# Performance work log

Hardware: AMD Instinct MI355X
Metric: run time of the kernel (lower is better)

The kernel has to match this reference:

```python
import jax, jax.numpy as jnp
import numpy as np
import math

FACTOR = 5


def setup_inputs() -> dict:
    key = jax.random.key(0)
    k1, k2, k3, k4 = jax.random.split(key, 4)
    B, L, H, D = 4, 2048, 8, 64
    sample_k = FACTOR * int(np.ceil(np.log(L)))  # 40
    queries = jax.random.normal(k1, (B, L, H, D), dtype=jnp.float32)
    keys = jax.random.normal(k2, (B, L, H, D), dtype=jnp.float32)
    values = jax.random.normal(k3, (B, L, H, D), dtype=jnp.float32)
    # per-query sampled key indices (replaces the host-side random.sample loop)
    index_sample = jax.random.randint(k4, (L, sample_k), 0, L, dtype=jnp.int64)
    return {"queries": queries, "keys": keys, "values": values,
            "index_sample": index_sample}


def reference(queries, keys, values, index_sample):
    B, L_Q, H, D = queries.shape
    L_K = keys.shape[1]
    # [B, L, H, D] -> [B, H, L, D]
    Q = jnp.transpose(queries, (0, 2, 1, 3))
    K = jnp.transpose(keys, (0, 2, 1, 3))
    V = jnp.transpose(values, (0, 2, 1, 3))

    u = min(FACTOR * int(np.ceil(np.log(L_Q))), L_Q)  # n_top

    # --- _prob_QK: sample-score-topk-gather ---
    # K_sample[b,h,i,s,e] = K[b,h,index_sample[i,s],e]  -> [B,H,L_Q,S,E]
    K_sample = K[:, :, index_sample, :]
    Q_K_sample = jnp.einsum('bhie,bhise->bhis', Q, K_sample)  # [B,H,L_Q,S]
    M = Q_K_sample.max(axis=-1) - Q_K_sample.sum(axis=-1) / L_K  # [B,H,L_Q]
    _, M_top = jax.lax.top_k(M, u)  # [B,H,u] indices of sparse queries

    Q_reduce = jnp.take_along_axis(Q, M_top[..., None], axis=2)  # [B,H,u,D]
    scores = jnp.einsum('bhue,bhke->bhuk', Q_reduce, K)  # [B,H,u,L_K]

    scale = 1.0 / math.sqrt(D)
    scores = scores * scale

    # --- initial context (mask_flag=True): causal running sum of V ---
    context = jnp.cumsum(V, axis=2)  # [B,H,L_Q,D]

    # --- ProbMask: causal mask rows gathered at M_top ---
    causal_mask = jnp.arange(L_K)[None, None, None, :] > M_top[..., None]
    scores = jnp.where(causal_mask, -jnp.inf, scores)
    attn = jax.nn.softmax(scores, axis=-1)  # [B,H,u,L_K]

    update = jnp.einsum('bhuk,bhkd->bhud', attn, V)  # [B,H,u,D]
    bi = jnp.arange(B)[:, None, None]
    hi = jnp.arange(H)[None, :, None]
    context = context.at[bi, hi, M_top].set(update)

    # back to [B, L, H, D]
    return jnp.transpose(context, (0, 2, 1, 3))
```

## Files before the change

kernel.cpp:

```cpp
#include <hip/hip_runtime.h>
#include <hip/hip_bf16.h>
#include <math.h>


#define BB 4
#define LL 2048
#define HH 8
#define DD 64
#define SS 40
#define UU 40
#define CC 64
#define LC (LL/CC)

#define KC    64
#define NCH2  8
#define UG    2
#define KSUB  4
#define KPAD  68
#define PPAD  68

__attribute__((amdgpu_waves_per_eu(4, 8)))
__global__ void k_measure(const float* __restrict__ Q, const float* __restrict__ K,
                          const int* __restrict__ idx, float* __restrict__ M)
{
    int tid  = threadIdx.x;
    int lane = tid & 63;
    int wave = tid >> 6;
    int qid  = blockIdx.x * 4 + wave;
    int bh = qid / LL;  int i = qid - bh * LL;
    int b  = bh / HH;   int h = bh - b * HH;

    int sg = lane >> 4;
    int d4 = lane & 15;

    const float* qrow = Q + (((size_t)b * LL + i) * HH + h) * DD;
    float4 qv = *(const float4*)(qrow + d4 * 4);

    const float* Kh = K + ((size_t)b * LL * HH + h) * DD;
    const int* ip = idx + (size_t)i * SS;
    const size_t RS = (size_t)HH * DD;

    int kk0 = ip[0*4+sg], kk1 = ip[1*4+sg], kk2 = ip[2*4+sg], kk3 = ip[3*4+sg];
    int kk4 = ip[4*4+sg], kk5 = ip[5*4+sg], kk6 = ip[6*4+sg], kk7 = ip[7*4+sg];
    int kk8 = ip[8*4+sg], kk9 = ip[9*4+sg];
    float4 kv0 = *(const float4*)(Kh + (size_t)kk0 * RS + d4 * 4);
    float4 kv1 = *(const float4*)(Kh + (size_t)kk1 * RS + d4 * 4);
    float4 kv2 = *(const float4*)(Kh + (size_t)kk2 * RS + d4 * 4);
    float4 kv3 = *(const float4*)(Kh + (size_t)kk3 * RS + d4 * 4);
    float4 kv4 = *(const float4*)(Kh + (size_t)kk4 * RS + d4 * 4);
    float4 kv5 = *(const float4*)(Kh + (size_t)kk5 * RS + d4 * 4);
    float4 kv6 = *(const float4*)(Kh + (size_t)kk6 * RS + d4 * 4);
    float4 kv7 = *(const float4*)(Kh + (size_t)kk7 * RS + d4 * 4);
    float4 kv8 = *(const float4*)(Kh + (size_t)kk8 * RS + d4 * 4);
    float4 kv9 = *(const float4*)(Kh + (size_t)kk9 * RS + d4 * 4);

#define DOT4(kv) (fmaf(qv.w, kv.w, fmaf(qv.z, kv.z, fmaf(qv.y, kv.y, qv.x * kv.x))))
    float p0 = DOT4(kv0), p1 = DOT4(kv1), p2 = DOT4(kv2), p3 = DOT4(kv3);
    float p4 = DOT4(kv4), p5 = DOT4(kv5), p6 = DOT4(kv6), p7 = DOT4(kv7);
    float p8 = DOT4(kv8), p9 = DOT4(kv9);
#undef DOT4

#define RED(off) \
    p0 += __shfl_xor(p0, off); p1 += __shfl_xor(p1, off); \
    p2 += __shfl_xor(p2, off); p3 += __shfl_xor(p3, off); \
    p4 += __shfl_xor(p4, off); p5 += __shfl_xor(p5, off); \
    p6 += __shfl_xor(p6, off); p7 += __shfl_xor(p7, off); \
    p8 += __shfl_xor(p8, off); p9 += __shfl_xor(p9, off);
    RED(1) RED(2) RED(4) RED(8)
#undef RED

    float maxv = fmaxf(fmaxf(fmaxf(p0, p1), fmaxf(p2, p3)),
                       fmaxf(fmaxf(p4, p5), fmaxf(fmaxf(p6, p7), fmaxf(p8, p9))));
    float sumv = ((p0 + p1) + (p2 + p3)) + ((p4 + p5) + (p6 + p7)) + (p8 + p9);

    maxv = fmaxf(maxv, __shfl_xor(maxv, 16));
    sumv += __shfl_xor(sumv, 16);
    maxv = fmaxf(maxv, __shfl_xor(maxv, 32));
    sumv += __shfl_xor(sumv, 32);

    if (lane == 0) M[qid] = maxv - sumv * (1.0f / (float)LL);
}

__global__ void k_topk(const float* __restrict__ M, int* __restrict__ topIdx)
{
    int lane = threadIdx.x;
    int bh   = blockIdx.x;
    const float* Mp = M + (size_t)bh * LL;

    unsigned k[32];
    #pragma unroll
    for (int r = 0; r < 32; ++r) {
        unsigned u = __float_as_uint(Mp[r * 64 + lane]);
        k[r] = (u & 0x80000000u) ? ~u : (u | 0x80000000u);
    }

    unsigned T = 0u;
    for (int bit = 31; bit >= 0; --bit) {
        unsigned cand = T | (1u << bit);
        int c = 0;
        #pragma unroll
        for (int r = 0; r < 32; ++r) c += (k[r] >= cand) ? 1 : 0;
        #pragma unroll
        for (int off = 1; off < 64; off <<= 1) c += __shfl_xor(c, off);
        if (c >= UU) T = cand;
    }

    int cGT = 0, cGE = 0;
    #pragma unroll
    for (int r = 0; r < 32; ++r) {
        cGT += (k[r] > T) ? 1 : 0;
        cGE += (k[r] >= T) ? 1 : 0;
    }
    #pragma unroll
    for (int off = 1; off < 64; off <<= 1) {
        cGT += __shfl_xor(cGT, off);
        cGE += __shfl_xor(cGE, off);
    }

    int need = UU - cGT;
    int X = LL;
    if (cGE - cGT != need) {
        int lo2 = 0;
        for (int bit = 10; bit >= 0; --bit) {
            int cand = lo2 | (1 << bit);
            int c = 0;
            #pragma unroll
            for (int r = 0; r < 32; ++r)
                c += (k[r] == T && (r * 64 + lane) < cand) ? 1 : 0;
            #pragma unroll
            for (int off = 1; off < 64; off <<= 1) c += __shfl_xor(c, off);
            if (c < need) lo2 = cand;
        }
        X = lo2 + 1;
    }

    unsigned inMask = 0u;
    int cnt = 0;
    #pragma unroll
    for (int r = 0; r < 32; ++r) {
        bool in = (k[r] > T) || (k[r] == T && (r * 64 + lane) < X);
        if (in) { inMask |= 1u << r; ++cnt; }
    }
    int pre = cnt;
    #pragma unroll
    for (int off = 1; off < 64; off <<= 1) {
        int v = __shfl_up(pre, off);
        if (lane >= off) pre += v;
    }
    int slot = pre - cnt;
    #pragma unroll
    for (int r = 0; r < 32; ++r) {
        if ((inMask >> r) & 1u) {
            topIdx[bh * UU + slot] = r * 64 + lane;
            ++slot;
        }
    }
}

__launch_bounds__(256, 2)
__global__ void k_attn(const float* __restrict__ Q, const float* __restrict__ K,
                       const float* __restrict__ V, const int* __restrict__ topIdx,
                       float* __restrict__ Oc, float* __restrict__ Lc)
{
    __shared__ float sK[2][KC][KPAD];
    __shared__ float sV[2][KC][KPAD];
    __shared__ float sP[20][PPAD];
    __shared__ int   sPos[UU];

    int t   = threadIdx.x;
    int bid = blockIdx.x;
    int bh  = bid / (NCH2 * UG);
    int rem = bid % (NCH2 * UG);
    int ch  = rem / UG, ug = rem % UG;
    int b   = bh / HH, h = bh % HH;

    if (t < UU) sPos[t] = topIdx[bh * UU + t];

    int j  = t & 63;
    int w  = t >> 6, lane = t & 63;
    int ub = __builtin_amdgcn_readfirstlane(w) * 5;

    int d4p = t & 15, tg = t >> 4;
    float4 a0 = {0,0,0,0}, a1 = {0,0,0,0};
    float den[5] = {0.f, 0.f, 0.f, 0.f, 0.f};

    const float* Kh = K + ((size_t)b * LL * HH + h) * DD;
    const float* Vh = V + ((size_t)b * LL * HH + h) * DD;

    float4 pk0, pk1, pk2, pk3, pv0, pv1, pv2, pv3;

#define ISSUE(k0_) { \
    size_t g0 = (size_t)((k0_) +  0 + tg) * (HH * DD) + d4p * 4; \
    size_t g1 = (size_t)((k0_) + 16 + tg) * (HH * DD) + d4p * 4; \
    size_t g2 = (size_t)((k0_) + 32 + tg) * (HH * DD) + d4p * 4; \
    size_t g3 = (size_t)((k0_) + 48 + tg) * (HH * DD) + d4p * 4; \
    pk0 = *(const float4*)(Kh + g0); pv0 = *(const float4*)(Vh + g0); \
    pk1 = *(const float4*)(Kh + g1); pv1 = *(const float4*)(Vh + g1); \
    pk2 = *(const float4*)(Kh + g2); pv2 = *(const float4*)(Vh + g2); \
    pk3 = *(const float4*)(Kh + g3); pv3 = *(const float4*)(Vh + g3); \
}
#define COMMIT(buf_) { \
    *(float4*)&sK[buf_][ 0 + tg][d4p * 4] = pk0; *(float4*)&sV[buf_][ 0 + tg][d4p * 4] = pv0; \
    *(float4*)&sK[buf_][16 + tg][d4p * 4] = pk1; *(float4*)&sV[buf_][16 + tg][d4p * 4] = pv1; \
    *(float4*)&sK[buf_][32 + tg][d4p * 4] = pk2; *(float4*)&sV[buf_][32 + tg][d4p * 4] = pv2; \
    *(float4*)&sK[buf_][48 + tg][d4p * 4] = pk3; *(float4*)&sV[buf_][48 + tg][d4p * 4] = pv3; \
}

    int k0base = ch * KSUB * KC;
    ISSUE(k0base);
    COMMIT(0);
    __syncthreads();

    #pragma unroll
    for (int sub = 0; sub < KSUB; ++sub) {
        int cur = sub & 1;
        int k0  = k0base + sub * KC;

        if (sub + 1 < KSUB) ISSUE(k0 + KC);

        int jg = k0 + j;
        {
            int p0 = __builtin_amdgcn_readfirstlane(sPos[ug * 20 + ub + 0]);
            int p1 = __builtin_amdgcn_readfirstlane(sPos[ug * 20 + ub + 1]);
            int p2 = __builtin_amdgcn_readfirstlane(sPos[ug * 20 + ub + 2]);
            int p3 = __builtin_amdgcn_readfirstlane(sPos[ug * 20 + ub + 3]);
            int p4 = __builtin_amdgcn_readfirstlane(sPos[ug * 20 + ub + 4]);
            const float* q0 = Q + (((size_t)b * LL + p0) * HH + h) * DD;
            const float* q1 = Q + (((size_t)b * LL + p1) * HH + h) * DD;
            const float* q2 = Q + (((size_t)b * LL + p2) * HH + h) * DD;
            const float* q3 = Q + (((size_t)b * LL + p3) * HH + h) * DD;
            const float* q4 = Q + (((size_t)b * LL + p4) * HH + h) * DD;
            float c0 = 0.f, c1 = 0.f, c2 = 0.f, c3 = 0.f, c4 = 0.f;
            #pragma unroll
            for (int d4 = 0; d4 < 16; ++d4) {
                float4 kk = *(const float4*)&sK[cur][j][d4 * 4];
                int d = d4 * 4;
                c0 = fmaf(kk.x, q0[d], c0); c0 = fmaf(kk.y, q0[d+1], c0);
                c0 = fmaf(kk.z, q0[d+2], c0); c0 = fmaf(kk.w, q0[d+3], c0);
                c1 = fmaf(kk.x, q1[d], c1); c1 = fmaf(kk.y, q1[d+1], c1);
                c1 = fmaf(kk.z, q1[d+2], c1); c1 = fmaf(kk.w, q1[d+3], c1);
                c2 = fmaf(kk.x, q2[d], c2); c2 = fmaf(kk.y, q2[d+1], c2);
                c2 = fmaf(kk.z, q2[d+2], c2); c2 = fmaf(kk.w, q2[d+3], c2);
                c3 = fmaf(kk.x, q3[d], c3); c3 = fmaf(kk.y, q3[d+1], c3);
                c3 = fmaf(kk.z, q3[d+2], c3); c3 = fmaf(kk.w, q3[d+3], c3);
                c4 = fmaf(kk.x, q4[d], c4); c4 = fmaf(kk.y, q4[d+1], c4);
                c4 = fmaf(kk.z, q4[d+2], c4); c4 = fmaf(kk.w, q4[d+3], c4);
            }
            float e0 = (jg > p0) ? 0.f : __expf(c0 * 0.125f);
            float e1 = (jg > p1) ? 0.f : __expf(c1 * 0.125f);
            float e2 = (jg > p2) ? 0.f : __expf(c2 * 0.125f);
            float e3 = (jg > p3) ? 0.f : __expf(c3 * 0.125f);
            float e4 = (jg > p4) ? 0.f : __expf(c4 * 0.125f);
            sP[ub + 0][j] = e0;
            sP[ub + 1][j] = e1;
            sP[ub + 2][j] = e2;
            sP[ub + 3][j] = e3;
            sP[ub + 4][j] = e4;
            #pragma unroll
            for (int off = 1; off < 64; off <<= 1) {
                e0 += __shfl_xor(e0, off);
                e1 += __shfl_xor(e1, off);
                e2 += __shfl_xor(e2, off);
                e3 += __shfl_xor(e3, off);
                e4 += __shfl_xor(e4, off);
            }
            den[0] += e0; den[1] += e1; den[2] += e2; den[3] += e3; den[4] += e4;
        }
        __syncthreads();

        if (sub + 1 < KSUB) {
            if (cur == 0) { COMMIT(1); } else { COMMIT(0); }
        }

        #pragma unroll 4
        for (int j4 = 0; j4 < KC / 4; ++j4) {
            float4 pj0 = *(const float4*)&sP[tg][j4 * 4];
            float4 pj1 = (tg < 4) ? *(const float4*)&sP[16 + tg][j4 * 4]
                                  : (float4){0,0,0,0};
            float4 va = *(const float4*)&sV[cur][j4 * 4 + 0][d4p * 4];
            float4 vb = *(const float4*)&sV[cur][j4 * 4 + 1][d4p * 4];
            float4 vc = *(const float4*)&sV[cur][j4 * 4 + 2][d4p * 4];
            float4 vd = *(const float4*)&sV[cur][j4 * 4 + 3][d4p * 4];
            a0.x = fmaf(pj0.x, va.x, fmaf(pj0.y, vb.x, fmaf(pj0.z, vc.x, fmaf(pj0.w, vd.x, a0.x))));
            a0.y = fmaf(pj0.x, va.y, fmaf(pj0.y, vb.y, fmaf(pj0.z, vc.y, fmaf(pj0.w, vd.y, a0.y))));
            a0.z = fmaf(pj0.x, va.z, fmaf(pj0.y, vb.z, fmaf(pj0.z, vc.z, fmaf(pj0.w, vd.z, a0.z))));
            a0.w = fmaf(pj0.x, va.w, fmaf(pj0.y, vb.w, fmaf(pj0.z, vc.w, fmaf(pj0.w, vd.w, a0.w))));
            a1.x = fmaf(pj1.x, va.x, fmaf(pj1.y, vb.x, fmaf(pj1.z, vc.x, fmaf(pj1.w, vd.x, a1.x))));
            a1.y = fmaf(pj1.x, va.y, fmaf(pj1.y, vb.y, fmaf(pj1.z, vc.y, fmaf(pj1.w, vd.y, a1.y))));
            a1.z = fmaf(pj1.x, va.z, fmaf(pj1.y, vb.z, fmaf(pj1.z, vc.z, fmaf(pj1.w, vd.z, a1.z))));
            a1.w = fmaf(pj1.x, va.w, fmaf(pj1.y, vb.w, fmaf(pj1.z, vc.w, fmaf(pj1.w, vd.w, a1.w))));
        }
        __syncthreads();
    }
#undef ISSUE
#undef COMMIT

    if (lane == 0) {
        int base = (bh * NCH2 + ch) * UU + ug * 20 + ub;
        Lc[base + 0] = den[0]; Lc[base + 1] = den[1]; Lc[base + 2] = den[2];
        Lc[base + 3] = den[3]; Lc[base + 4] = den[4];
    }
    {
        int u0g = ug * 20 + tg;
        size_t o0 = ((size_t)(bh * NCH2 + ch) * UU + u0g) * DD + d4p * 4;
        *(float4*)(Oc + o0) = a0;
        if (tg < 4) {
            int u1g = ug * 20 + 16 + tg;
            size_t o1 = ((size_t)(bh * NCH2 + ch) * UU + u1g) * DD + d4p * 4;
            *(float4*)(Oc + o1) = a1;
        }
    }
}

__global__ void k_chunksum(const float* __restrict__ V, float* __restrict__ chunkSum)
{
    int t  = threadIdx.x;
    int c  = blockIdx.x % CC;
    int bh = blockIdx.x / CC;
    int b  = bh / HH; int h = bh - b * HH;
    int d4 = t & 15, rs = t >> 4;

    float4 acc = {0,0,0,0};
    int l0 = c * LC;
    for (int l = l0 + rs; l < l0 + LC; l += 4) {
        float4 v = *(const float4*)(V + (((size_t)b * LL + l) * HH + h) * DD + d4 * 4);
        acc.x += v.x; acc.y += v.y; acc.z += v.z; acc.w += v.w;
    }
    acc.x += __shfl_xor(acc.x, 16); acc.y += __shfl_xor(acc.y, 16);
    acc.z += __shfl_xor(acc.z, 16); acc.w += __shfl_xor(acc.w, 16);
    acc.x += __shfl_xor(acc.x, 32); acc.y += __shfl_xor(acc.y, 32);
    acc.z += __shfl_xor(acc.z, 32); acc.w += __shfl_xor(acc.w, 32);
    if (t < 16)
        *(float4*)(chunkSum + ((size_t)bh * CC + c) * DD + d4 * 4) = acc;
}

__global__ void k_cumsum(const float* __restrict__ V, const float* __restrict__ chunkSum,
                         float* __restrict__ out)
{
    int t  = threadIdx.x;
    int c  = blockIdx.x & (CC - 1);
    int bh = blockIdx.x >> 6;
    int b  = bh / HH; int h = bh - b * HH;
    int d4 = t & 15, s = t >> 4;

    const float4* CS4 = (const float4*)chunkSum;
    float4 off = {0,0,0,0};
    for (int c2 = s; c2 < c; c2 += 4) {
        float4 x = CS4[((size_t)bh * CC + c2) * 16 + d4];
        off.x += x.x; off.y += x.y; off.z += x.z; off.w += x.w;
    }
    off.x += __shfl_xor(off.x, 16); off.y += __shfl_xor(off.y, 16);
    off.z += __shfl_xor(off.z, 16); off.w += __shfl_xor(off.w, 16);
    off.x += __shfl_xor(off.x, 32); off.y += __shfl_xor(off.y, 32);
    off.z += __shfl_xor(off.z, 32); off.w += __shfl_xor(off.w, 32);

    int l0 = c * LC + s * 8;
    size_t base = (((size_t)b * LL + l0) * HH + h) * DD + d4 * 4;
    const size_t stride = (size_t)HH * DD;

    float4 v[8];
    #pragma unroll
    for (int r = 0; r < 8; ++r)
        v[r] = *(const float4*)(V + base + (size_t)r * stride);
    #pragma unroll
    for (int r = 1; r < 8; ++r) {
        v[r].x += v[r-1].x; v[r].y += v[r-1].y;
        v[r].z += v[r-1].z; v[r].w += v[r-1].w;
    }

    float4 inc = v[7];
    float4 p1;
    p1.x = __shfl_up(inc.x, 16); p1.y = __shfl_up(inc.y, 16);
    p1.z = __shfl_up(inc.z, 16); p1.w = __shfl_up(inc.w, 16);
    if (s >= 1) { inc.x += p1.x; inc.y += p1.y; inc.z += p1.z; inc.w += p1.w; }
    float4 p2;
    p2.x = __shfl_up(inc.x, 32); p2.y = __shfl_up(inc.y, 32);
    p2.z = __shfl_up(inc.z, 32); p2.w = __shfl_up(inc.w, 32);
    if (s >= 2) { inc.x += p2.x; inc.y += p2.y; inc.z += p2.z; inc.w += p2.w; }

    float4 add;
    add.x = off.x + inc.x - v[7].x;
    add.y = off.y + inc.y - v[7].y;
    add.z = off.z + inc.z - v[7].z;
    add.w = off.w + inc.w - v[7].w;

    #pragma unroll
    for (int r = 0; r < 8; ++r) {
        float4 o;
        o.x = v[r].x + add.x; o.y = v[r].y + add.y;
        o.z = v[r].z + add.z; o.w = v[r].w + add.w;
        *(float4*)(out + base + (size_t)r * stride) = o;
    }
}

__global__ void k_finalize(const float* __restrict__ Oc, const float* __restrict__ Lc,
                           const int* __restrict__ topIdx, float* __restrict__ out)
{
    int bh = blockIdx.x;
    int b  = bh / HH, h = bh % HH;
    int t  = threadIdx.x;
    int d  = t & 63, w = t >> 6;
    for (int i = 0; i < 10; ++i) {
        int u = w * 10 + i;
        int pos = topIdx[bh * UU + u];
        float num = 0.f, den = 0.f;
        #pragma unroll
        for (int c = 0; c < NCH2; ++c) {
            num += Oc[((size_t)(bh * NCH2 + c) * UU + u) * DD + d];
            den += Lc[(bh * NCH2 + c) * UU + u];
        }
        out[(((size_t)b * LL + pos) * HH + h) * DD + d] = num / den;
    }
}

extern "C" void kernel_launch(void* const* d_in, const int* in_sizes, int n_in,
                              void* d_out, int out_size, void* d_ws, size_t ws_size,
                              hipStream_t stream)
{
    const float* Q   = (const float*)d_in[0];
    const float* K   = (const float*)d_in[1];
    const float* V   = (const float*)d_in[2];
    const int*   idx = (const int*)d_in[3];
    float* out = (float*)d_out;

    float* M        = (float*)d_ws;
    int*   topIdx   = (int*)(M + (size_t)BB * HH * LL);
    float* Oc       = (float*)(topIdx + BB * HH * UU);
    float* Lc       = Oc + (size_t)BB * HH * NCH2 * UU * DD;
    float* chunkSum = Lc + BB * HH * NCH2 * UU;

    k_measure <<<BB * HH * LL / 4,     256, 0, stream>>>(Q, K, idx, M);
    k_topk    <<<BB * HH,               64, 0, stream>>>(M, topIdx);
    k_attn    <<<BB * HH * NCH2 * UG, 256, 0, stream>>>(Q, K, V, topIdx, Oc, Lc);
    k_chunksum<<<BB * HH * CC,          64, 0, stream>>>(V, chunkSum);
    k_cumsum  <<<BB * HH * CC,          64, 0, stream>>>(V, chunkSum, out);
    k_finalize<<<BB * HH,              256, 0, stream>>>(Oc, Lc, topIdx, out);
}
```

Measured before the change: 182.1 us.

## Restructure k_measure to gather full key rows across all heads per query

The sparsity-measure kernel now assigns one block per (batch, query position) and handles all 8 heads together. Each sampled key row is read across every head as contiguous 2KB memory instead of 256B per-head fragments, and the index list is shared by all heads. Per-wave partial max/sum values are combined through shared memory with a barrier. The aim is to improve coalescing and cut redundant index loads, at the cost of a block-wide sync and a loop that serializes the reductions more.

```diff
diff --git a/kernel.cpp b/kernel.cpp
--- a/kernel.cpp
+++ b/kernel.cpp
@@ -19,66 +19,72 @@
 #define KPAD  68
 #define PPAD  68
 
-__attribute__((amdgpu_waves_per_eu(4, 8)))
 __global__ void k_measure(const float* __restrict__ Q, const float* __restrict__ K,
                           const int* __restrict__ idx, float* __restrict__ M)
 {
-    int tid  = threadIdx.x;
-    int lane = tid & 63;
-    int wave = tid >> 6;
-    int qid  = blockIdx.x * 4 + wave;
-    int bh = qid / LL;  int i = qid - bh * LL;
-    int b  = bh / HH;   int h = bh - b * HH;
-
-    int sg = lane >> 4;
-    int d4 = lane & 15;
-
-    const float* qrow = Q + (((size_t)b * LL + i) * HH + h) * DD;
-    float4 qv = *(const float4*)(qrow + d4 * 4);
-
-    const float* Kh = K + ((size_t)b * LL * HH + h) * DD;
-    const int* ip = idx + (size_t)i * SS;
-    const size_t RS = (size_t)HH * DD;
-
-    int kk0 = ip[0*4+sg], kk1 = ip[1*4+sg], kk2 = ip[2*4+sg], kk3 = ip[3*4+sg];
-    int kk4 = ip[4*4+sg], kk5 = ip[5*4+sg], kk6 = ip[6*4+sg], kk7 = ip[7*4+sg];
-    int kk8 = ip[8*4+sg], kk9 = ip[9*4+sg];
-    float4 kv0 = *(const float4*)(Kh + (size_t)kk0 * RS + d4 * 4);
-    float4 kv1 = *(const float4*)(Kh + (size_t)kk1 * RS + d4 * 4);
-    float4 kv2 = *(const float4*)(Kh + (size_t)kk2 * RS + d4 * 4);
-    float4 kv3 = *(const float4*)(Kh + (size_t)kk3 * RS + d4 * 4);
-    float4 kv4 = *(const float4*)(Kh + (size_t)kk4 * RS + d4 * 4);
-    float4 kv5 = *(const float4*)(Kh + (size_t)kk5 * RS + d4 * 4);
-    float4 kv6 = *(const float4*)(Kh + (size_t)kk6 * RS + d4 * 4);
-    float4 kv7 = *(const float4*)(Kh + (size_t)kk7 * RS + d4 * 4);
-    float4 kv8 = *(const float4*)(Kh + (size_t)kk8 * RS + d4 * 4);
-    float4 kv9 = *(const float4*)(Kh + (size_t)kk9 * RS + d4 * 4);
-
-#define DOT4(kv) (fmaf(qv.w, kv.w, fmaf(qv.z, kv.z, fmaf(qv.y, kv.y, qv.x * kv.x))))
-    float p0 = DOT4(kv0), p1 = DOT4(kv1), p2 = DOT4(kv2), p3 = DOT4(kv3);
-    float p4 = DOT4(kv4), p5 = DOT4(kv5), p6 = DOT4(kv6), p7 = DOT4(kv7);
-    float p8 = DOT4(kv8), p9 = DOT4(kv9);
+    __shared__ float sMax[4][8];
+    __shared__ float sSum[4][8];
+
+    int t   = threadIdx.x;
+    int blk = blockIdx.x;
+    int b   = blk >> 11;
+    int i   = blk & (LL - 1);
+    int w    = t >> 6, lane = t & 63;
+    int hg   = lane >> 4;
+    int d4   = lane & 15;
+
+    const int*   ip   = idx + (size_t)i * SS + w * 10;
+    const float* Kb   = K + (size_t)b * (LL * HH * DD);
+    const float* Qrow = Q + ((size_t)b * LL + i) * (HH * DD);
+
+    float4 qa = *(const float4*)(Qrow + hg * DD + d4 * 4);
+    float4 qb = *(const float4*)(Qrow + (4 + hg) * DD + d4 * 4);
+
+    float maxa = -INFINITY, suma = 0.f;
+    float maxb = -INFINITY, sumb = 0.f;
+
+#define DOT4(q_, k_) (fmaf((q_).w, (k_).w, fmaf((q_).z, (k_).z, \
+                      fmaf((q_).y, (k_).y, (q_).x * (k_).x))))
+    #pragma unroll
+    for (int u = 0; u < 10; u += 2) {
+        int k0 = ip[u], k1 = ip[u + 1];
+        const float* r0 = Kb + (size_t)k0 * (HH * DD);
+        const float* r1 = Kb + (size_t)k1 * (HH * DD);
+        float4 a0 = *(const float4*)(r0 + hg * DD + d4 * 4);
+        float4 b0 = *(const float4*)(r0 + (4 + hg) * DD + d4 * 4);
+        float4 a1 = *(const float4*)(r1 + hg * DD + d4 * 4);
+        float4 b1 = *(const float4*)(r1 + (4 + hg) * DD + d4 * 4);
+
+        float pa0 = DOT4(qa, a0), pb0 = DOT4(qb, b0);
+        float pa1 = DOT4(qa, a1), pb1 = DOT4(qb, b1);
+
+        #pragma unroll
+        for (int off = 1; off < 16; off <<= 1) {
+            pa0 += __shfl_xor(pa0, off);
+            pb0 += __shfl_xor(pb0, off);
+            pa1 += __shfl_xor(pa1, off);
+            pb1 += __shfl_xor(pb1, off);
+        }
+        maxa = fmaxf(maxa, fmaxf(pa0, pa1));  suma += pa0 + pa1;
+        maxb = fmaxf(maxb, fmaxf(pb0, pb1));  sumb += pb0 + pb1;
+    }
 #undef DOT4
 
-#define RED(off) \
-    p0 += __shfl_xor(p0, off); p1 += __shfl_xor(p1, off); \
-    p2 += __shfl_xor(p2, off); p3 += __shfl_xor(p3, off); \
-    p4 += __shfl_xor(p4, off); p5 += __shfl_xor(p5, off); \
-    p6 += __shfl_xor(p6, off); p7 += __shfl_xor(p7, off); \
-    p8 += __shfl_xor(p8, off); p9 += __shfl_xor(p9, off);
-    RED(1) RED(2) RED(4) RED(8)
-#undef RED
-
-    float maxv = fmaxf(fmaxf(fmaxf(p0, p1), fmaxf(p2, p3)),
-                       fmaxf(fmaxf(p4, p5), fmaxf(fmaxf(p6, p7), fmaxf(p8, p9))));
-    float sumv = ((p0 + p1) + (p2 + p3)) + ((p4 + p5) + (p6 + p7)) + (p8 + p9);
-
-    maxv = fmaxf(maxv, __shfl_xor(maxv, 16));
-    sumv += __shfl_xor(sumv, 16);
-    maxv = fmaxf(maxv, __shfl_xor(maxv, 32));
-    sumv += __shfl_xor(sumv, 32);
-
-    if (lane == 0) M[qid] = maxv - sumv * (1.0f / (float)LL);
+    if (d4 == 0) {
+        sMax[w][hg]     = maxa;  sSum[w][hg]     = suma;
+        sMax[w][4 + hg] = maxb;  sSum[w][4 + hg] = sumb;
+    }
+    __syncthreads();
+
+    if (t < 8) {
+        float mx = sMax[0][t], sm = sSum[0][t];
+        #pragma unroll
+        for (int w2 = 1; w2 < 4; ++w2) {
+            mx = fmaxf(mx, sMax[w2][t]);
+            sm += sSum[w2][t];
+        }
+        M[((size_t)(b * HH + t)) * LL + i] = mx - sm * (1.0f / (float)LL);
+    }
 }
 
 __global__ void k_topk(const float* __restrict__ M, int* __restrict__ topIdx)
@@ -429,10 +435,10 @@
     float* Lc       = Oc + (size_t)BB * HH * NCH2 * UU * DD;
     float* chunkSum = Lc + BB * HH * NCH2 * UU;
 
-    k_measure <<<BB * HH * LL / 4,     256, 0, stream>>>(Q, K, idx, M);
-    k_topk    <<<BB * HH,               64, 0, stream>>>(M, topIdx);
+    k_measure <<<BB * LL,             256, 0, stream>>>(Q, K, idx, M);
+    k_topk    <<<BB * HH,              64, 0, stream>>>(M, topIdx);
     k_attn    <<<BB * HH * NCH2 * UG, 256, 0, stream>>>(Q, K, V, topIdx, Oc, Lc);
-    k_chunksum<<<BB * HH * CC,          64, 0, stream>>>(V, chunkSum);
-    k_cumsum  <<<BB * HH * CC,          64, 0, stream>>>(V, chunkSum, out);
-    k_finalize<<<BB * HH,              256, 0, stream>>>(Oc, Lc, topIdx, out);
-}
+    k_chunksum<<<BB * HH * CC,         64, 0, stream>>>(V, chunkSum);
+    k_cumsum  <<<BB * HH * CC,         64, 0, stream>>>(V, chunkSum, out);
+    k_finalize<<<BB * HH,             256, 0, stream>>>(Oc, Lc, topIdx, out);
+}
```

Result: slower. 186.7 us (+2.5%).
